# Optimization experiments

Hardware: AMD Instinct MI355X
Metric: run time of the kernel (lower is better)

Reference implementation:

```python
import jax, jax.numpy as jnp
import numpy as np

M, IN_F, OUT_F = 32, 8192, 32768
ACT_QMAX = 127.0  # act_bits=8


def unpack_int4(w_packed, in_features):
    # w_packed: (out, in//2) int32 holding two int4 nibbles per byte
    lower = w_packed & 15
    upper = (w_packed >> 4) & 15
    # sign-extend 4-bit values: v - ((v & 8) << 1) maps 8..15 -> -8..-1
    lower = lower - ((lower & 8) << 1)
    upper = upper - ((upper & 8) << 1)
    w = jnp.stack([lower, upper], axis=-1).reshape(w_packed.shape[0], -1)
    return w[:, :in_features]


def setup_inputs() -> dict:
    key = jax.random.key(0)
    k1, k2, k3, k4, k5 = jax.random.split(key, 5)
    x = jax.random.normal(k1, (M, IN_F), dtype=jnp.float32)
    # random packed bytes in [0, 256): every value is a valid pair of int4 nibbles
    weight_packed = jax.random.randint(k2, (OUT_F, IN_F // 2), 0, 256, dtype=jnp.int32)
    weight_scale = jax.random.uniform(k3, (OUT_F, 1), dtype=jnp.float32) * 0.01 + 1e-4
    act_scale = jax.random.uniform(k4, (1,), dtype=jnp.float32) * 0.1 + 0.01
    bias = jax.random.normal(k5, (OUT_F,), dtype=jnp.float32)
    return {"x": x, "weight_packed": weight_packed, "weight_scale": weight_scale,
            "act_scale": act_scale, "bias": bias}


def reference(x, weight_packed, weight_scale, act_scale, bias):
    # 1) static input quantization (round + clamp to int8 range, kept in fp32)
    x_q = jnp.clip(jnp.round(x / act_scale), -ACT_QMAX, ACT_QMAX)
    # 2) unpack int4 weights and emulate GEMM in fp32 (as the original does)
    w = unpack_int4(weight_packed, x.shape[-1]).astype(jnp.float32)  # (out, in)
    y_q = jnp.einsum('mi,oi->mo', x_q, w)  # (M, out)
    # 3) dequant: act_scale * per-channel weight_scale, then bias
    y = y_q * (act_scale * weight_scale.T)  # weight_scale.T: (1, out)
    y = y + bias[None, :]
    return y
```

## Files before the change

kernel.cpp:

```cpp
#include <hip/hip_runtime.h>
#include <hip/hip_bf16.h>
#include <stdint.h>

#define M_DIM  32
#define IN_FEAT 8192
#define OUT_FEAT 32768
#define KSPLIT 4
#define KSLICE (IN_FEAT / KSPLIT)

typedef __attribute__((ext_vector_type(8))) __bf16 bf16x8;
typedef __attribute__((ext_vector_type(4))) float f32x4;
typedef __attribute__((ext_vector_type(4))) int   i32x4;
typedef __attribute__((ext_vector_type(8))) unsigned short u16x8;

__global__ void quant_kernel(const float* __restrict__ x,
                             const float* __restrict__ act_scale,
                             unsigned short* __restrict__ xq) {
  int i = blockIdx.x * blockDim.x + threadIdx.x;
  float s = act_scale[0];
  float q = rintf(x[i] / s);
  q = fminf(fmaxf(q, -127.0f), 127.0f);
  unsigned int u = __builtin_bit_cast(unsigned int, q);
  xq[i] = (unsigned short)(u >> 16);
}

__global__ __launch_bounds__(256) void gemm_kernel(
    const unsigned short* __restrict__ xq,
    const int*   __restrict__ wp,
    const float* __restrict__ wscale,
    const float* __restrict__ act_scale,
    const float* __restrict__ bias,
    float* __restrict__ out)
{
  const int lane  = threadIdx.x & 63;
  const int wave  = threadIdx.x >> 6;
  const int l15   = lane & 15;
  const int krow  = lane >> 4;

  const int kslice = blockIdx.x & (KSPLIT - 1);
  const int nblk   = blockIdx.x >> 2;
  const int n      = (nblk << 6) + (wave << 4) + l15;

  const int kbase = kslice * KSLICE;
  const int k0    = kbase + krow * 8;

  const u16x8* a0p = (const u16x8*)(xq + (size_t)l15        * IN_FEAT);
  const u16x8* a1p = (const u16x8*)(xq + (size_t)(l15 + 16) * IN_FEAT);
  const i32x4* bp  = (const i32x4*)(wp + (size_t)n * (IN_FEAT / 2));

  f32x4 acc0 = {0.f, 0.f, 0.f, 0.f};
  f32x4 acc1 = {0.f, 0.f, 0.f, 0.f};

#pragma unroll 4
  for (int k = k0; k < kbase + KSLICE; k += 32) {
    u16x8 a0u = a0p[k >> 3];
    u16x8 a1u = a1p[k >> 3];
    i32x4 w4 = __builtin_nontemporal_load(&bp[k >> 3]);

    union { unsigned int u[4]; bf16x8 v; } bu;
#pragma unroll
    for (int j = 0; j < 4; ++j) {
      int v  = w4[j];
      int lo = ((v & 15) ^ 8) - 8;
      int hi = (((v >> 4) & 15) ^ 8) - 8;
      unsigned int ulo = __builtin_bit_cast(unsigned int, (float)lo);
      unsigned int uhi = __builtin_bit_cast(unsigned int, (float)hi);
      bu.u[j] = (ulo >> 16) | (uhi & 0xFFFF0000u);
    }

    bf16x8 a0 = __builtin_bit_cast(bf16x8, a0u);
    bf16x8 a1 = __builtin_bit_cast(bf16x8, a1u);
    acc0 = __builtin_amdgcn_mfma_f32_16x16x32_bf16(a0, bu.v, acc0, 0, 0, 0);
    acc1 = __builtin_amdgcn_mfma_f32_16x16x32_bf16(a1, bu.v, acc1, 0, 0, 0);
  }

  const float sc = act_scale[0] * wscale[n];
  const float bs = bias[n];
  const int m0 = krow * 4;
#pragma unroll
  for (int r = 0; r < 4; ++r) {
    float v0 = acc0[r] * sc;
    float v1 = acc1[r] * sc;
    if (kslice == 0) { v0 += bs; v1 += bs; }
    atomicAdd(out + (size_t)(m0 + r)      * OUT_FEAT + n, v0);
    atomicAdd(out + (size_t)(m0 + r + 16) * OUT_FEAT + n, v1);
  }
}

extern "C" void kernel_launch(void* const* d_in, const int* in_sizes, int n_in,
                              void* d_out, int out_size, void* d_ws, size_t ws_size,
                              hipStream_t stream) {
  const float* x      = (const float*)d_in[0];
  const int*   wp     = (const int*)  d_in[1];
  const float* wscale = (const float*)d_in[2];
  const float* ascale = (const float*)d_in[3];
  const float* bias   = (const float*)d_in[4];
  float* out = (float*)d_out;
  unsigned short* xq = (unsigned short*)d_ws;

  hipMemsetAsync(out, 0, (size_t)M_DIM * OUT_FEAT * sizeof(float), stream);
  quant_kernel<<<(M_DIM * IN_FEAT) / 256, 256, 0, stream>>>(x, ascale, xq);
  gemm_kernel<<<(OUT_FEAT / 64) * KSPLIT, 256, 0, stream>>>(xq, wp, wscale, ascale, bias, out);
}
```

Before: 796.1 us.

## Switch GEMM to int8 MFMA with nibble-shift unpack and split-K reduce kernel

Activations are quantized to packed int8 instead of bf16. Int4 weights are unpacked into int8 values scaled by 16 using shifts and perm, and fed to the i32 16x16x64 int8 MFMA, so each instruction covers twice the K of the old bf16 path. Float atomics and the memset are replaced by per-k-slice int32 partial buffers plus a separate reduce kernel that applies scales (with a 1/16 correction) and bias. The loop also gains software prefetch of the next iteration's loads. This costs an extra launch and partial-buffer traffic (about 16MB written and read back).

```diff
diff --git a/kernel.cpp b/kernel.cpp
--- a/kernel.cpp
+++ b/kernel.cpp
@@ -1,90 +1,128 @@
 #include <hip/hip_runtime.h>
-#include <hip/hip_bf16.h>
 #include <stdint.h>
+
 
 #define M_DIM  32
 #define IN_FEAT 8192
 #define OUT_FEAT 32768
 #define KSPLIT 4
 #define KSLICE (IN_FEAT / KSPLIT)
+#define NITER  (KSLICE / 64)
 
-typedef __attribute__((ext_vector_type(8))) __bf16 bf16x8;
+typedef __attribute__((ext_vector_type(4))) int   i32x4;
 typedef __attribute__((ext_vector_type(4))) float f32x4;
-typedef __attribute__((ext_vector_type(4))) int   i32x4;
-typedef __attribute__((ext_vector_type(8))) unsigned short u16x8;
 
-__global__ void quant_kernel(const float* __restrict__ x,
-                             const float* __restrict__ act_scale,
-                             unsigned short* __restrict__ xq) {
+__global__ __launch_bounds__(256) void quant_kernel(
+    const float* __restrict__ x,
+    const float* __restrict__ act_scale,
+    int* __restrict__ xq4) {
   int i = blockIdx.x * blockDim.x + threadIdx.x;
   float s = act_scale[0];
-  float q = rintf(x[i] / s);
-  q = fminf(fmaxf(q, -127.0f), 127.0f);
-  unsigned int u = __builtin_bit_cast(unsigned int, q);
-  xq[i] = (unsigned short)(u >> 16);
+  f32x4 v = ((const f32x4*)x)[i];
+  int r = 0;
+#pragma unroll
+  for (int j = 0; j < 4; ++j) {
+    float q = rintf(v[j] / s);
+    q = fminf(fmaxf(q, -127.0f), 127.0f);
+    r |= ((int)q & 0xFF) << (8 * j);
+  }
+  xq4[i] = r;
+}
+
+__device__ __forceinline__ int unpack2(int v) {
+  return ((v << 4) | (v << 8)) & 0xF0F0;
 }
 
 __global__ __launch_bounds__(256) void gemm_kernel(
-    const unsigned short* __restrict__ xq,
-    const int*   __restrict__ wp,
+    const char* __restrict__ xq,
+    const int*  __restrict__ wp,
+    int* __restrict__ partial)
+{
+  const int lane = threadIdx.x & 63;
+  const int wave = threadIdx.x >> 6;
+  const int l15  = lane & 15;
+  const int krow = lane >> 4;
+
+  const int kslice = blockIdx.x & (KSPLIT - 1);
+  const int nblk   = blockIdx.x >> 2;
+  const int n      = (nblk << 6) + (wave << 4) + l15;
+  const int kbase  = kslice * KSLICE;
+
+  const i32x4* a0p = (const i32x4*)(xq + (size_t)l15        * IN_FEAT + kbase);
+  const i32x4* a1p = (const i32x4*)(xq + (size_t)(l15 + 16) * IN_FEAT + kbase);
+  const i32x4* bp  = (const i32x4*)((const char*)(wp + (size_t)n * (IN_FEAT / 2))
+                                    + (size_t)kbase * 2);
+
+  i32x4 acc0 = {0, 0, 0, 0};
+  i32x4 acc1 = {0, 0, 0, 0};
+
+  i32x4 w_lo = __builtin_nontemporal_load(&bp[krow * 2]);
+  i32x4 w_hi = __builtin_nontemporal_load(&bp[krow * 2 + 1]);
+  i32x4 a0   = a0p[krow];
+  i32x4 a1   = a1p[krow];
+
+#pragma unroll 2
+  for (int i = 0; i < NITER; ++i) {
+    const int ip = (i + 1 < NITER) ? (i + 1) : (NITER - 1);
+    i32x4 w_lo_n = __builtin_nontemporal_load(&bp[ip * 8 + krow * 2]);
+    i32x4 w_hi_n = __builtin_nontemporal_load(&bp[ip * 8 + krow * 2 + 1]);
+    i32x4 a0_n   = a0p[ip * 4 + krow];
+    i32x4 a1_n   = a1p[ip * 4 + krow];
+
+    int p0 = unpack2(w_lo[0]);
+    int p1 = unpack2(w_lo[1]);
+    int p2 = unpack2(w_lo[2]);
+    int p3 = unpack2(w_lo[3]);
+    int p4 = unpack2(w_hi[0]);
+    int p5 = unpack2(w_hi[1]);
+    int p6 = unpack2(w_hi[2]);
+    int p7 = unpack2(w_hi[3]);
+    i32x4 bfrag;
+    bfrag[0] = __builtin_amdgcn_perm(p1, p0, 0x05040100);
+    bfrag[1] = __builtin_amdgcn_perm(p3, p2, 0x05040100);
+    bfrag[2] = __builtin_amdgcn_perm(p5, p4, 0x05040100);
+    bfrag[3] = __builtin_amdgcn_perm(p7, p6, 0x05040100);
+
+    acc0 = __builtin_amdgcn_mfma_i32_16x16x64_i8(a0, bfrag, acc0, 0, 0, 0);
+    acc1 = __builtin_amdgcn_mfma_i32_16x16x64_i8(a1, bfrag, acc1, 0, 0, 0);
+
+    w_lo = w_lo_n; w_hi = w_hi_n; a0 = a0_n; a1 = a1_n;
+  }
+
+  int* pout = partial + (size_t)kslice * (M_DIM * OUT_FEAT);
+  const int m0 = krow * 4;
+#pragma unroll
+  for (int r = 0; r < 4; ++r) {
+    __builtin_nontemporal_store(acc0[r], &pout[(size_t)(m0 + r)      * OUT_FEAT + n]);
+    __builtin_nontemporal_store(acc1[r], &pout[(size_t)(m0 + r + 16) * OUT_FEAT + n]);
+  }
+}
+
+__global__ __launch_bounds__(256) void reduce_kernel(
+    const int*   __restrict__ partial,
     const float* __restrict__ wscale,
     const float* __restrict__ act_scale,
     const float* __restrict__ bias,
     float* __restrict__ out)
 {
-  const int lane  = threadIdx.x & 63;
-  const int wave  = threadIdx.x >> 6;
-  const int l15   = lane & 15;
-  const int krow  = lane >> 4;
+  const int t  = blockIdx.x * blockDim.x + threadIdx.x;
+  const int m  = t >> 13;
+  const int n4 = (t & 8191) << 2;
+  const size_t off = (size_t)m * OUT_FEAT + n4;
 
-  const int kslice = blockIdx.x & (KSPLIT - 1);
-  const int nblk   = blockIdx.x >> 2;
-  const int n      = (nblk << 6) + (wave << 4) + l15;
+  i32x4 s = *(const i32x4*)(partial + off);
+#pragma unroll
+  for (int k = 1; k < KSPLIT; ++k)
+    s += *(const i32x4*)(partial + (size_t)k * (M_DIM * OUT_FEAT) + off);
 
-  const int kbase = kslice * KSLICE;
-  const int k0    = kbase + krow * 8;
-
-  const u16x8* a0p = (const u16x8*)(xq + (size_t)l15        * IN_FEAT);
-  const u16x8* a1p = (const u16x8*)(xq + (size_t)(l15 + 16) * IN_FEAT);
-  const i32x4* bp  = (const i32x4*)(wp + (size_t)n * (IN_FEAT / 2));
-
-  f32x4 acc0 = {0.f, 0.f, 0.f, 0.f};
-  f32x4 acc1 = {0.f, 0.f, 0.f, 0.f};
-
-#pragma unroll 4
-  for (int k = k0; k < kbase + KSLICE; k += 32) {
-    u16x8 a0u = a0p[k >> 3];
-    u16x8 a1u = a1p[k >> 3];
-    i32x4 w4 = __builtin_nontemporal_load(&bp[k >> 3]);
-
-    union { unsigned int u[4]; bf16x8 v; } bu;
+  const float as = act_scale[0] * (1.0f / 16.0f);
+  f32x4 ws = *(const f32x4*)(wscale + n4);
+  f32x4 bs = *(const f32x4*)(bias + n4);
+  f32x4 r;
 #pragma unroll
-    for (int j = 0; j < 4; ++j) {
-      int v  = w4[j];
-      int lo = ((v & 15) ^ 8) - 8;
-      int hi = (((v >> 4) & 15) ^ 8) - 8;
-      unsigned int ulo = __builtin_bit_cast(unsigned int, (float)lo);
-      unsigned int uhi = __builtin_bit_cast(unsigned int, (float)hi);
-      bu.u[j] = (ulo >> 16) | (uhi & 0xFFFF0000u);
-    }
-
-    bf16x8 a0 = __builtin_bit_cast(bf16x8, a0u);
-    bf16x8 a1 = __builtin_bit_cast(bf16x8, a1u);
-    acc0 = __builtin_amdgcn_mfma_f32_16x16x32_bf16(a0, bu.v, acc0, 0, 0, 0);
-    acc1 = __builtin_amdgcn_mfma_f32_16x16x32_bf16(a1, bu.v, acc1, 0, 0, 0);
-  }
-
-  const float sc = act_scale[0] * wscale[n];
-  const float bs = bias[n];
-  const int m0 = krow * 4;
-#pragma unroll
-  for (int r = 0; r < 4; ++r) {
-    float v0 = acc0[r] * sc;
-    float v1 = acc1[r] * sc;
-    if (kslice == 0) { v0 += bs; v1 += bs; }
-    atomicAdd(out + (size_t)(m0 + r)      * OUT_FEAT + n, v0);
-    atomicAdd(out + (size_t)(m0 + r + 16) * OUT_FEAT + n, v1);
-  }
+  for (int j = 0; j < 4; ++j)
+    r[j] = (float)s[j] * (as * ws[j]) + bs[j];
+  *(f32x4*)(out + off) = r;
 }
 
 extern "C" void kernel_launch(void* const* d_in, const int* in_sizes, int n_in,
@@ -96,9 +134,11 @@
   const float* ascale = (const float*)d_in[3];
   const float* bias   = (const float*)d_in[4];
   float* out = (float*)d_out;
-  unsigned short* xq = (unsigned short*)d_ws;
 
-  hipMemsetAsync(out, 0, (size_t)M_DIM * OUT_FEAT * sizeof(float), stream);
-  quant_kernel<<<(M_DIM * IN_FEAT) / 256, 256, 0, stream>>>(x, ascale, xq);
-  gemm_kernel<<<(OUT_FEAT / 64) * KSPLIT, 256, 0, stream>>>(xq, wp, wscale, ascale, bias, out);
+  int*  partial = (int*)d_ws;
+  char* xq      = (char*)d_ws + (size_t)KSPLIT * M_DIM * OUT_FEAT * sizeof(int);
+
+  quant_kernel<<<(M_DIM * IN_FEAT / 4) / 256, 256, 0, stream>>>(x, ascale, (int*)xq);
+  gemm_kernel<<<(OUT_FEAT / 64) * KSPLIT, 256, 0, stream>>>(xq, wp, partial);
+  reduce_kernel<<<(M_DIM * OUT_FEAT / 4) / 256, 256, 0, stream>>>(partial, wscale, ascale, bias, out);
 }
```

Result: faster. 730.2 us (-8.3%).
